# Performance work log

Measured on AMD Instinct MI355X. Metric: run time of the kernel, lower is better.

The kernel has to match this reference:

```python
import jax, jax.numpy as jnp
import numpy as np
from jax import lax

N, T, I, H = 32, 2048, 512, 1024

def setup_inputs() -> dict:
    key = jax.random.key(0)
    k1, k2, k3, k4 = jax.random.split(key, 4)
    x = jax.random.normal(k1, (N, T, I), dtype=jnp.float32)
    # nn.Linear(in, out): weight (out, in), bias (out,)
    s_ih = 1.0 / np.sqrt(I)
    s_hh = 1.0 / np.sqrt(H)
    w_ih = jax.random.uniform(k2, (H, I), jnp.float32, -s_ih, s_ih)
    b_ih = jax.random.uniform(k3, (H,), jnp.float32, -s_ih, s_ih)
    w_hh = jax.random.uniform(k4, (H, H), jnp.float32, -s_hh, s_hh)
    return {"x": x, "w_ih": w_ih, "b_ih": b_ih, "w_hh": w_hh}

def reference(x, w_ih, b_ih, w_hh):
    # Precompute input projections for all timesteps: (N, T, H)
    proj = jnp.einsum('nti,hi->nth', x, w_ih) + b_ih
    h0 = proj[:, 0]  # hidden_0 = W_ih(x[:,0])  (N, H)

    def step(h, u):
        # hidden_t = W_hh @ hidden_{t-1} + W_ih(x[:, t-1])  (note t-1, per source)
        h = h @ w_hh.T + u
        return h, h

    # For t = 1..T-1 the input term uses proj[:, t-1] -> proj[:, 0:T-1]
    us = jnp.swapaxes(proj[:, :T - 1], 0, 1)  # (T-1, N, H)
    _, hs = lax.scan(step, h0, us)            # (T-1, N, H)
    hiddens = jnp.concatenate([h0[None], hs], axis=0)  # (T, N, H)
    out = jnp.swapaxes(hiddens, 0, 1)         # (N, T, H)
    return (out, out)
```

## Files before the change

### kernel.cpp

```cpp
#include <hip/hip_runtime.h>
#include <hip/hip_bf16.h>
#include <stdint.h>

#define TT 2048
#define NB 32
#define II 512
#define HH 1024
#define CC 8
#define MCH 256
#define RR 8192

typedef __attribute__((ext_vector_type(8))) short short8;
typedef __attribute__((ext_vector_type(4))) short short4v;
typedef __attribute__((ext_vector_type(4))) float f32x4;

__device__ __forceinline__ float b2f(short s) {
    union { unsigned u; float f; } x;
    x.u = ((unsigned)(unsigned short)s) << 16;
    return x.f;
}
__device__ __forceinline__ short f2b(float f) {
    unsigned u = __float_as_uint(f);
    u += 0x7fff + ((u >> 16) & 1);
    return (short)(u >> 16);
}

__device__ __forceinline__ void async16(const void* g, const void* l) {
    __builtin_amdgcn_global_load_lds(
        (const __attribute__((address_space(1))) void*)g,
        (__attribute__((address_space(3))) void*)l, 16, 0, 0);
}

__global__ void cvt_kernel(const float* __restrict__ s, short* __restrict__ d, long n4) {
    long i = (long)blockIdx.x * blockDim.x + threadIdx.x;
    if (i < n4) {
        float4 v = ((const float4*)s)[i];
        short4v o;
        o.x = f2b(v.x); o.y = f2b(v.y); o.z = f2b(v.z); o.w = f2b(v.w);
        *(short4v*)(d + 4 * i) = o;
    }
}

__global__ void transpose_kernel(const short* __restrict__ s, short* __restrict__ d) {
    __shared__ short tile[32][33];
    int tx = threadIdx.x & 31, ty = threadIdx.x >> 5;
    int bx = blockIdx.x * 32, by = blockIdx.y * 32;
    for (int y = ty; y < 32; y += 8) tile[y][tx] = s[(long)(by + y) * HH + bx + tx];
    __syncthreads();
    for (int y = ty; y < 32; y += 8) d[(long)(bx + y) * HH + by + tx] = tile[tx][y];
}

__global__ void seed_kernel(const short* __restrict__ projb, short* __restrict__ sbuf1) {
    int r = blockIdx.x;
    int i = r >> 5, n = r & 31;
    int c0 = threadIdx.x * 4;
    short4v v = *(const short4v*)(projb + ((long)(n * TT + i * CC)) * HH + c0);
    *(short4v*)(sbuf1 + (long)r * HH + c0) = v;
}

__global__ void prep_kernel(const short* __restrict__ projb, const short* __restrict__ SC,
                            short* __restrict__ sh1, short* __restrict__ sh2) {
    int r = blockIdx.x;
    int i = r >> 5, n = r & 31;
    int c0 = threadIdx.x * 4;
    short4v z = {0, 0, 0, 0};
    short4v p0 = *(const short4v*)(projb + ((long)n * TT) * HH + c0);
    short4v v1 = (i == 0) ? p0 : *(const short4v*)(SC + ((long)((i - 1) * NB + n)) * HH + c0);
    short4v v2 = (i == 0) ? z : ((i == 1) ? p0 : *(const short4v*)(SC + ((long)((i - 2) * NB + n)) * HH + c0));
    *(short4v*)(sh1 + (long)r * HH + c0) = v1;
    *(short4v*)(sh2 + (long)r * HH + c0) = v2;
}

template<int BN, int SRC_MODE, bool BIAS, int NF32, bool WB16>
__global__ __launch_bounds__(256) void gemm_bt(
    const short* __restrict__ A, const short* __restrict__ B, int K,
    const void* src, const float* __restrict__ bias,
    float* f0, float* f1, short* __restrict__ bd,
    int dsI, int dsN, int doff, int ssI, int ssN, int soff)
{
    constexpr int NJ = BN / 32;
    __shared__ __align__(16) short As[128 * 32];
    __shared__ __align__(16) short Bs[BN * 32];
    const int tid = threadIdx.x;
    const int wave = tid >> 6, lane = tid & 63;
    const int wm = wave & 1, wn = wave >> 1;
    const int quad = lane >> 4, l16 = lane & 15;
    const long row0 = (long)blockIdx.x * 128, col0 = (long)blockIdx.y * BN;

    const short* ag = A + (row0 + (tid >> 2)) * K + (tid & 3) * 8;
    const short* bg = B + (col0 + (tid >> 2)) * K + (tid & 3) * 8;
    short* la = As + wave * 512;
    short* lb = Bs + wave * 512;
    const long k64 = (long)64 * K;

    f32x4 zero = {0.f, 0.f, 0.f, 0.f};
    f32x4 acc[4][NJ];
#pragma unroll
    for (int i = 0; i < 4; i++)
#pragma unroll
        for (int j = 0; j < NJ; j++) acc[i][j] = zero;

    for (int kk = 0; kk < K; kk += 32) {
        __syncthreads();
        async16(ag + kk,       la);
        async16(ag + kk + k64, la + 2048);
        async16(bg + kk,       lb);
        if constexpr (BN == 128)
            async16(bg + kk + k64, lb + 2048);
        __syncthreads();

        short8 af[4], bf[NJ];
#pragma unroll
        for (int i = 0; i < 4; i++)
            af[i] = *(const short8*)(As + (wm * 64 + i * 16 + l16) * 32 + quad * 8);
#pragma unroll
        for (int j = 0; j < NJ; j++)
            bf[j] = *(const short8*)(Bs + (wn * (BN / 2) + j * 16 + l16) * 32 + quad * 8);
#pragma unroll
        for (int i = 0; i < 4; i++)
#pragma unroll
            for (int j = 0; j < NJ; j++)
                acc[i][j] = __builtin_amdgcn_mfma_f32_16x16x32_bf16(af[i], bf[j], acc[i][j], 0, 0, 0);
    }

#pragma unroll
    for (int i = 0; i < 4; i++) {
#pragma unroll
        for (int j = 0; j < NJ; j++) {
            const int col = (int)col0 + wn * (BN / 2) + j * 16 + l16;
            float bv = 0.f;
            if (BIAS) bv = bias[col];
#pragma unroll
            for (int v = 0; v < 4; v++) {
                const int row = (int)row0 + wm * 64 + i * 16 + quad * 4 + v;
                float val = acc[i][j][v] + bv;
                if (SRC_MODE == 1) {
                    const long sr = (long)(row >> 5) * ssI + (long)(row & 31) * ssN + soff;
                    val += b2f(((const short*)src)[sr * HH + col]);
                }
                if (NF32 >= 1) {
                    const long dr = (long)(row >> 5) * dsI + (long)(row & 31) * dsN + doff;
                    f0[dr * HH + col] = val;
                    if (NF32 == 2) f1[dr * HH + col] = val;
                }
                if (WB16) bd[(long)row * HH + col] = f2b(val);
            }
        }
    }
}

extern "C" void kernel_launch(void* const* d_in, const int* in_sizes, int n_in,
                              void* d_out, int out_size, void* d_ws, size_t ws_size,
                              hipStream_t stream)
{
    const float* x   = (const float*)d_in[0];
    const float* wih = (const float*)d_in[1];
    const float* bih = (const float*)d_in[2];
    const float* whh = (const float*)d_in[3];
    float* out0 = (float*)d_out;
    float* out1 = out0 + (long)NB * TT * HH;

    char* p = (char*)d_ws;
    auto alloc = [&](size_t bytes) -> char* {
        char* r = p;
        p += (bytes + 255) & ~(size_t)255;
        return r;
    };
    short* projb = (short*)alloc((size_t)NB * TT * HH * 2);
    short* wihb  = (short*)alloc((size_t)HH * II * 2);
    short* whhb  = (short*)alloc((size_t)HH * HH * 2);
    short* powT  = (short*)alloc((size_t)HH * HH * 2);
    short* powA  = (short*)alloc((size_t)HH * HH * 2);
    short* powB  = (short*)alloc((size_t)HH * HH * 2);
    short* xb    = (short*)alloc((size_t)NB * TT * II * 2);
    const size_t SB = (size_t)RR * HH * 2;
    char* ov = (char*)xb;
    short* sbuf0 = (short*)(ov + 0 * SB);
    short* sbuf1 = (short*)(ov + 1 * SB);
    short* SCb   = (short*)(ov + 2 * SB);
    short* hbuf0 = (short*)(ov + 3 * SB);
    short* sh1   = sbuf0;
    short* sh2   = sbuf1;
    short* hbuf1 = SCb;

    dim3 blk(256);
    const dim3 sg(RR / 128, HH / 64);

    long n4x = (long)NB * TT * II / 4;
    cvt_kernel<<<dim3((unsigned)((n4x + 255) / 256)), blk, 0, stream>>>(x, xb, n4x);
    long n4a = (long)HH * II / 4;
    cvt_kernel<<<dim3((unsigned)((n4a + 255) / 256)), blk, 0, stream>>>(wih, wihb, n4a);
    long n4b = (long)HH * HH / 4;
    cvt_kernel<<<dim3((unsigned)((n4b + 255) / 256)), blk, 0, stream>>>(whh, whhb, n4b);

    gemm_bt<128, 0, true, 0, true><<<dim3(512, 8), blk, 0, stream>>>(
        xb, wihb, II, nullptr, bih, nullptr, nullptr, projb, 0, 0, 0, 0, 0, 0);

    dim3 tg(32, 32);
    dim3 pg(8, 16);
    transpose_kernel<<<tg, blk, 0, stream>>>(whhb, powT);
    gemm_bt<64, 0, false, 0, true><<<pg, blk, 0, stream>>>(
        whhb, powT, HH, nullptr, nullptr, nullptr, nullptr, powA, 0, 0, 0, 0, 0, 0);
    transpose_kernel<<<tg, blk, 0, stream>>>(powA, powT);
    gemm_bt<64, 0, false, 0, true><<<pg, blk, 0, stream>>>(
        powA, powT, HH, nullptr, nullptr, nullptr, nullptr, powB, 0, 0, 0, 0, 0, 0);
    transpose_kernel<<<tg, blk, 0, stream>>>(powB, powT);
    gemm_bt<64, 0, false, 0, true><<<pg, blk, 0, stream>>>(
        powB, powT, HH, nullptr, nullptr, nullptr, nullptr, powA, 0, 0, 0, 0, 0, 0);

    seed_kernel<<<dim3(RR), blk, 0, stream>>>(projb, sbuf1);

    for (int c = 2; c <= CC; ++c) {
        const short* a = (c & 1) ? sbuf0 : sbuf1;
        short* o = (c < CC) ? ((c & 1) ? sbuf1 : sbuf0) : SCb;
        gemm_bt<64, 1, false, 0, true><<<sg, blk, 0, stream>>>(
            a, whhb, HH, projb, nullptr, nullptr, nullptr, o,
            0, 0, 0, CC, TT, c - 1);
    }

    prep_kernel<<<dim3(RR), blk, 0, stream>>>(projb, SCb, sh1, sh2);
    gemm_bt<64, 1, false, 2, true><<<sg, blk, 0, stream>>>(
        sh2, powA, HH, sh1, nullptr, out0, out1, hbuf0,
        CC, TT, 0, NB, 1, 0);

    for (int c = 1; c < CC; ++c) {
        const short* a = ((c - 1) & 1) ? hbuf1 : hbuf0;
        short* o = (c & 1) ? hbuf1 : hbuf0;
        gemm_bt<64, 1, false, 2, true><<<sg, blk, 0, stream>>>(
            a, whhb, HH, projb, nullptr, out0, out1, o,
            CC, TT, c, CC, TT, c - 1);
    }
}
```

Measured before the change: 1.457 ms.

## Replace sequential per-chunk recurrence with one batched GEMM against stacked W powers

Builds a stacked matrix of W_hh powers (W^0..W^7) and applies it in a single wide GEMM from the chunk-start hidden states. This replaces the seven dependent per-step GEMMs in the final phase, accumulating onto the partial sums already written to the output. The chunk-local partials are now written to out0 during the first phase. The GEMM k-loop also gets double-buffered LDS staging, and the main GEMMs move to 128-wide N tiles. The trade-off is extra power-matrix GEMMs and read-modify-write traffic on the fp32 outputs, plus more bf16 rounding error from the higher powers.

```diff
diff --git a/kernel.cpp b/kernel.cpp
--- a/kernel.cpp
+++ b/kernel.cpp
@@ -50,12 +50,16 @@
     for (int y = ty; y < 32; y += 8) d[(long)(bx + y) * HH + by + tx] = tile[tx][y];
 }
 
-__global__ void seed_kernel(const short* __restrict__ projb, short* __restrict__ sbuf1) {
+__global__ void seed_kernel(const short* __restrict__ projb, short* __restrict__ sbuf1,
+                            float* __restrict__ out0) {
     int r = blockIdx.x;
     int i = r >> 5, n = r & 31;
     int c0 = threadIdx.x * 4;
     short4v v = *(const short4v*)(projb + ((long)(n * TT + i * CC)) * HH + c0);
     *(short4v*)(sbuf1 + (long)r * HH + c0) = v;
+    float4 f;
+    f.x = b2f(v.x); f.y = b2f(v.y); f.z = b2f(v.z); f.w = b2f(v.w);
+    *(float4*)(out0 + ((long)(n * TT + i * CC + 1)) * HH + c0) = f;
 }
 
 __global__ void prep_kernel(const short* __restrict__ projb, const short* __restrict__ SC,
@@ -71,7 +75,7 @@
     *(short4v*)(sh2 + (long)r * HH + c0) = v2;
 }
 
-template<int BN, int SRC_MODE, bool BIAS, int NF32, bool WB16>
+template<int BN, int SRC, bool BIAS, int NF32, int WMODE>
 __global__ __launch_bounds__(256) void gemm_bt(
     const short* __restrict__ A, const short* __restrict__ B, int K,
     const void* src, const float* __restrict__ bias,
@@ -79,8 +83,10 @@
     int dsI, int dsN, int doff, int ssI, int ssN, int soff)
 {
     constexpr int NJ = BN / 32;
-    __shared__ __align__(16) short As[128 * 32];
-    __shared__ __align__(16) short Bs[BN * 32];
+    __shared__ __align__(16) short As0[128 * 32];
+    __shared__ __align__(16) short As1[128 * 32];
+    __shared__ __align__(16) short Bs0[BN * 32];
+    __shared__ __align__(16) short Bs1[BN * 32];
     const int tid = threadIdx.x;
     const int wave = tid >> 6, lane = tid & 63;
     const int wm = wave & 1, wn = wave >> 1;
@@ -89,9 +95,16 @@
 
     const short* ag = A + (row0 + (tid >> 2)) * K + (tid & 3) * 8;
     const short* bg = B + (col0 + (tid >> 2)) * K + (tid & 3) * 8;
-    short* la = As + wave * 512;
-    short* lb = Bs + wave * 512;
     const long k64 = (long)64 * K;
+    const int lw = wave * 512;
+
+    auto STAGE = [&](short* Asb, short* Bsb, int kk) {
+        async16(ag + kk,       Asb + lw);
+        async16(ag + kk + k64, Asb + lw + 2048);
+        async16(bg + kk,       Bsb + lw);
+        if constexpr (BN == 128)
+            async16(bg + kk + k64, Bsb + lw + 2048);
+    };
 
     f32x4 zero = {0.f, 0.f, 0.f, 0.f};
     f32x4 acc[4][NJ];
@@ -100,50 +113,63 @@
 #pragma unroll
         for (int j = 0; j < NJ; j++) acc[i][j] = zero;
 
-    for (int kk = 0; kk < K; kk += 32) {
-        __syncthreads();
-        async16(ag + kk,       la);
-        async16(ag + kk + k64, la + 2048);
-        async16(bg + kk,       lb);
-        if constexpr (BN == 128)
-            async16(bg + kk + k64, lb + 2048);
-        __syncthreads();
-
+    auto COMPUTE = [&](const short* Asb, const short* Bsb) {
         short8 af[4], bf[NJ];
 #pragma unroll
         for (int i = 0; i < 4; i++)
-            af[i] = *(const short8*)(As + (wm * 64 + i * 16 + l16) * 32 + quad * 8);
+            af[i] = *(const short8*)(Asb + (wm * 64 + i * 16 + l16) * 32 + quad * 8);
 #pragma unroll
         for (int j = 0; j < NJ; j++)
-            bf[j] = *(const short8*)(Bs + (wn * (BN / 2) + j * 16 + l16) * 32 + quad * 8);
+            bf[j] = *(const short8*)(Bsb + (wn * (BN / 2) + j * 16 + l16) * 32 + quad * 8);
 #pragma unroll
         for (int i = 0; i < 4; i++)
 #pragma unroll
             for (int j = 0; j < NJ; j++)
                 acc[i][j] = __builtin_amdgcn_mfma_f32_16x16x32_bf16(af[i], bf[j], acc[i][j], 0, 0, 0);
+    };
+
+    const int nt = K / 32;
+    STAGE(As0, Bs0, 0);
+    __syncthreads();
+    for (int t = 0; t < nt; t += 2) {
+        STAGE(As1, Bs1, (t + 1) * 32);
+        COMPUTE(As0, Bs0);
+        __syncthreads();
+        if (t + 2 < nt) STAGE(As0, Bs0, (t + 2) * 32);
+        COMPUTE(As1, Bs1);
+        __syncthreads();
     }
 
 #pragma unroll
     for (int i = 0; i < 4; i++) {
 #pragma unroll
         for (int j = 0; j < NJ; j++) {
-            const int col = (int)col0 + wn * (BN / 2) + j * 16 + l16;
+            const int colg = (int)col0 + wn * (BN / 2) + j * 16 + l16;
+            const int page = colg >> 10;
+            const int colp = colg & 1023;
             float bv = 0.f;
-            if (BIAS) bv = bias[col];
+            if (BIAS) bv = bias[colg];
 #pragma unroll
             for (int v = 0; v < 4; v++) {
                 const int row = (int)row0 + wm * 64 + i * 16 + quad * 4 + v;
                 float val = acc[i][j][v] + bv;
-                if (SRC_MODE == 1) {
+                if constexpr (SRC == 1) {
                     const long sr = (long)(row >> 5) * ssI + (long)(row & 31) * ssN + soff;
-                    val += b2f(((const short*)src)[sr * HH + col]);
+                    val += b2f(((const short*)src)[sr * HH + colg]);
                 }
-                if (NF32 >= 1) {
+                if constexpr (SRC == 2) {
+                    const long dr = (long)(row >> 5) * dsI + (long)(row & 31) * dsN + doff + page;
+                    val += f0[dr * HH + colp];
+                    f0[dr * HH + colp] = val;
+                    f1[dr * HH + colp] = val;
+                } else if constexpr (NF32 >= 1) {
                     const long dr = (long)(row >> 5) * dsI + (long)(row & 31) * dsN + doff;
-                    f0[dr * HH + col] = val;
-                    if (NF32 == 2) f1[dr * HH + col] = val;
+                    f0[dr * HH + colg] = val;
+                    if constexpr (NF32 == 2) f1[dr * HH + colg] = val;
                 }
-                if (WB16) bd[(long)row * HH + col] = f2b(val);
+                if constexpr (WMODE == 1) bd[(long)row * HH + colg] = f2b(val);
+                else if constexpr (WMODE == 2)
+                    bd[(long)page * (HH * HH) + (long)row * HH + colp] = f2b(val);
             }
         }
     }
@@ -169,22 +195,21 @@
     short* projb = (short*)alloc((size_t)NB * TT * HH * 2);
     short* wihb  = (short*)alloc((size_t)HH * II * 2);
     short* whhb  = (short*)alloc((size_t)HH * HH * 2);
-    short* powT  = (short*)alloc((size_t)HH * HH * 2);
-    short* powA  = (short*)alloc((size_t)HH * HH * 2);
-    short* powB  = (short*)alloc((size_t)HH * HH * 2);
     short* xb    = (short*)alloc((size_t)NB * TT * II * 2);
     const size_t SB = (size_t)RR * HH * 2;
     char* ov = (char*)xb;
-    short* sbuf0 = (short*)(ov + 0 * SB);
-    short* sbuf1 = (short*)(ov + 1 * SB);
-    short* SCb   = (short*)(ov + 2 * SB);
-    short* hbuf0 = (short*)(ov + 3 * SB);
-    short* sh1   = sbuf0;
-    short* sh2   = sbuf1;
-    short* hbuf1 = SCb;
+    short* sbuf0  = (short*)(ov + 0 * SB);
+    short* sbuf1  = (short*)(ov + 1 * SB);
+    short* SCb    = (short*)(ov + 2 * SB);
+    short* hbuf0  = (short*)(ov + 3 * SB);
+    short* sh1    = sbuf0;
+    short* sh2    = sbuf1;
+    short* powcat = SCb;
+    short* powsT  = (short*)out1;
+    const long PG = (long)HH * HH;
 
     dim3 blk(256);
-    const dim3 sg(RR / 128, HH / 64);
+    const dim3 sg(RR / 128, HH / 128);
 
     long n4x = (long)NB * TT * II / 4;
     cvt_kernel<<<dim3((unsigned)((n4x + 255) / 256)), blk, 0, stream>>>(x, xb, n4x);
@@ -193,41 +218,45 @@
     long n4b = (long)HH * HH / 4;
     cvt_kernel<<<dim3((unsigned)((n4b + 255) / 256)), blk, 0, stream>>>(whh, whhb, n4b);
 
-    gemm_bt<128, 0, true, 0, true><<<dim3(512, 8), blk, 0, stream>>>(
+    gemm_bt<128, 0, true, 0, 1><<<dim3(512, 8), blk, 0, stream>>>(
         xb, wihb, II, nullptr, bih, nullptr, nullptr, projb, 0, 0, 0, 0, 0, 0);
 
+    seed_kernel<<<dim3(RR), blk, 0, stream>>>(projb, sbuf1, out0);
+
+    for (int c = 2; c < CC; ++c) {
+        const short* a = (c & 1) ? sbuf0 : sbuf1;
+        short* o = (c & 1) ? sbuf1 : sbuf0;
+        gemm_bt<128, 1, false, 1, 1><<<sg, blk, 0, stream>>>(
+            a, whhb, HH, projb, nullptr, out0, nullptr, o,
+            CC, TT, c, CC, TT, c - 1);
+    }
+    gemm_bt<128, 1, false, 0, 1><<<sg, blk, 0, stream>>>(
+        sbuf1, whhb, HH, projb, nullptr, nullptr, nullptr, SCb,
+        0, 0, 0, CC, TT, CC - 1);
+
+    prep_kernel<<<dim3(RR), blk, 0, stream>>>(projb, SCb, sh1, sh2);
+
     dim3 tg(32, 32);
-    dim3 pg(8, 16);
-    transpose_kernel<<<tg, blk, 0, stream>>>(whhb, powT);
-    gemm_bt<64, 0, false, 0, true><<<pg, blk, 0, stream>>>(
-        whhb, powT, HH, nullptr, nullptr, nullptr, nullptr, powA, 0, 0, 0, 0, 0, 0);
-    transpose_kernel<<<tg, blk, 0, stream>>>(powA, powT);
-    gemm_bt<64, 0, false, 0, true><<<pg, blk, 0, stream>>>(
-        powA, powT, HH, nullptr, nullptr, nullptr, nullptr, powB, 0, 0, 0, 0, 0, 0);
-    transpose_kernel<<<tg, blk, 0, stream>>>(powB, powT);
-    gemm_bt<64, 0, false, 0, true><<<pg, blk, 0, stream>>>(
-        powB, powT, HH, nullptr, nullptr, nullptr, nullptr, powA, 0, 0, 0, 0, 0, 0);
-
-    seed_kernel<<<dim3(RR), blk, 0, stream>>>(projb, sbuf1);
-
-    for (int c = 2; c <= CC; ++c) {
-        const short* a = (c & 1) ? sbuf0 : sbuf1;
-        short* o = (c < CC) ? ((c & 1) ? sbuf1 : sbuf0) : SCb;
-        gemm_bt<64, 1, false, 0, true><<<sg, blk, 0, stream>>>(
-            a, whhb, HH, projb, nullptr, nullptr, nullptr, o,
-            0, 0, 0, CC, TT, c - 1);
-    }
-
-    prep_kernel<<<dim3(RR), blk, 0, stream>>>(projb, SCb, sh1, sh2);
-    gemm_bt<64, 1, false, 2, true><<<sg, blk, 0, stream>>>(
-        sh2, powA, HH, sh1, nullptr, out0, out1, hbuf0,
+    cvt_kernel<<<dim3((unsigned)((n4b + 255) / 256)), blk, 0, stream>>>(whh, powcat, n4b);
+    transpose_kernel<<<tg, blk, 0, stream>>>(whhb, powsT);
+    gemm_bt<64, 0, false, 0, 2><<<dim3(8, 16), blk, 0, stream>>>(
+        whhb, powsT, HH, nullptr, nullptr, nullptr, nullptr, powcat + 1 * PG,
+        0, 0, 0, 0, 0, 0);
+    transpose_kernel<<<tg, blk, 0, stream>>>(powcat + 1 * PG, powsT + 1 * PG);
+    gemm_bt<64, 0, false, 0, 2><<<dim3(8, 32), blk, 0, stream>>>(
+        powcat + 1 * PG, powsT, HH, nullptr, nullptr, nullptr, nullptr, powcat + 2 * PG,
+        0, 0, 0, 0, 0, 0);
+    transpose_kernel<<<tg, blk, 0, stream>>>(powcat + 2 * PG, powsT + 2 * PG);
+    transpose_kernel<<<tg, blk, 0, stream>>>(powcat + 3 * PG, powsT + 3 * PG);
+    gemm_bt<64, 0, false, 0, 2><<<dim3(8, 64), blk, 0, stream>>>(
+        powcat + 3 * PG, powsT, HH, nullptr, nullptr, nullptr, nullptr, powcat + 4 * PG,
+        0, 0, 0, 0, 0, 0);
+
+    gemm_bt<128, 1, false, 2, 1><<<sg, blk, 0, stream>>>(
+        sh2, powcat + 7 * PG, HH, sh1, nullptr, out0, out1, hbuf0,
         CC, TT, 0, NB, 1, 0);
 
-    for (int c = 1; c < CC; ++c) {
-        const short* a = ((c - 1) & 1) ? hbuf1 : hbuf0;
-        short* o = (c & 1) ? hbuf1 : hbuf0;
-        gemm_bt<64, 1, false, 2, true><<<sg, blk, 0, stream>>>(
-            a, whhb, HH, projb, nullptr, out0, out1, o,
-            CC, TT, c, CC, TT, c - 1);
-    }
-}
+    gemm_bt<128, 2, false, 2, 0><<<dim3(RR / 128, (CC - 1) * HH / 128), blk, 0, stream>>>(
+        hbuf0, powcat, HH, nullptr, nullptr, out0, out1, nullptr,
+        CC, TT, 1, 0, 0, 0);
+}
```

New measurement: 1.568 ms. 7.6% more time.
